# Kernel optimization log

Hardware: AMD Instinct MI355X
Metric: run time of the kernel (lower is better)

Reference implementation:

```python
import jax, jax.numpy as jnp
import numpy as np

B, U, H, M, D = 64, 1024, 16, 512, 4  # batch, units, numheads, memsize, depth
HS = U // H  # headsize


def setup_inputs() -> dict:
    key = jax.random.key(0)
    ks = jax.random.split(key, 6)
    scale = 0.02
    return {
        "x": jax.random.normal(ks[0], (B, U), jnp.float32),
        "memory": jax.random.normal(ks[1], (B, M * U), jnp.float32),
        "Wr": jax.random.normal(ks[2], (D, U, H * (M + 1)), jnp.float32) * scale,
        "br": jnp.zeros((D, H * (M + 1)), jnp.float32),
        "Ww": jax.random.normal(ks[3], (D, U, H * M), jnp.float32) * scale,
        "bw": jnp.zeros((D, H * M), jnp.float32),
        "Wk": jax.random.normal(ks[4], (D, U, U), jnp.float32) * scale,
        "bk": jnp.zeros((D, U), jnp.float32),
    }


def reference(x, memory, Wr, br, Ww, bw, Wk, bk):
    b = x.shape[0]
    mem4 = memory.reshape(b, M, H, HS)          # [B, M, H, HS]
    out = x
    for l in range(D):  # fixed small depth loop over structurally distinct layers
        inp4 = out.reshape(b, 1, H, HS)
        att = jnp.concatenate([mem4, inp4], axis=1)        # [B, M+1, H, HS]
        memstate = att.reshape(b, M + 1, U).mean(axis=1)   # [B, U]
        # read attention: per-head softmax over memory slots (+input slot)
        rlog = memstate @ Wr[l] + br[l]                    # [B, H*(M+1)]
        rw = jax.nn.softmax(rlog.reshape(b, M + 1, H), axis=1)  # [B, M+1, H]
        att = att * rw[..., None]                          # weighted read
        newval = jax.nn.relu(att.reshape(b, M + 1, U).sum(axis=1) @ Wk[l] + bk[l])  # [B, U]
        # write attention: per-head softmax over memory slots
        wlog = newval @ Ww[l] + bw[l]                      # [B, H*M]
        ww = jax.nn.softmax(wlog.reshape(b, M, H), axis=1)[..., None]  # [B, M, H, 1]
        mem4 = (1.0 - ww) * mem4 + ww * newval.reshape(b, 1, H, HS)
        out = newval
    return out, mem4.reshape(b, M * U)
```

## Files before the change

kernel.cpp:

```cpp
#include <hip/hip_runtime.h>

#define BB 64
#define UU 1024
#define HH 16
#define MM 512
#define DD 4
#define NR 8208
#define NW 8192
#define NK 1024

__device__ inline float warp_reduce_max(float v) {
    #pragma unroll
    for (int off = 32; off > 0; off >>= 1) v = fmaxf(v, __shfl_xor(v, off));
    return v;
}
__device__ inline float warp_reduce_sum(float v) {
    #pragma unroll
    for (int off = 32; off > 0; off >>= 1) v += __shfl_xor(v, off);
    return v;
}

__global__ void k_zero(float* __restrict__ p) {
    p[blockIdx.x * 256 + threadIdx.x] = 0.0f;
}

__global__ __launch_bounds__(256) void k_memsum(const float* __restrict__ mem,
                                                float* __restrict__ memsum) {
    const int b = blockIdx.x, mc = blockIdx.y, t = threadIdx.x;
    const float4* src = (const float4*)(mem + (size_t)b * MM * UU);
    float4 s = make_float4(0.f, 0.f, 0.f, 0.f);
    const int m0 = mc * 32;
    for (int m = m0; m < m0 + 32; ++m) {
        float4 v = src[(size_t)m * 256 + t];
        s.x += v.x; s.y += v.y; s.z += v.z; s.w += v.w;
    }
    float* d = memsum + b * UU + t * 4;
    atomicAdd(d + 0, s.x); atomicAdd(d + 1, s.y);
    atomicAdd(d + 2, s.z); atomicAdd(d + 3, s.w);
}

__global__ void k_prep_r(const float* __restrict__ memsum, const float* __restrict__ out,
                         float* __restrict__ memstate, float* __restrict__ wsum) {
    int i = blockIdx.x * 256 + threadIdx.x;
    memstate[i] = (memsum[i] + out[i]) * (1.0f / 513.0f);
    wsum[i] = 0.0f;
}

__global__ __launch_bounds__(256) void k_gemm(const float* __restrict__ A,
                                              const float* __restrict__ W,
                                              float* __restrict__ pbuf,
                                              int N, int kchunk, int kcl2 ) {
    __shared__ float At[256 * 64];
    const int t = threadIdx.x;
    const int cb = blockIdx.x * 128;
    const int ks = blockIdx.y;
    const int kbase = ks * kchunk;

    const int n4 = kchunk >> 4;
    const int kq_mask = (kchunk >> 2) - 1;
    for (int i = 0; i < n4; ++i) {
        int idx4 = t + (i << 8);
        int r = idx4 >> kcl2;
        int kq = idx4 & kq_mask;
        float4 v = *(const float4*)(A + r * UU + kbase + (kq << 2));
        int kk = kq << 2;
        At[(kk + 0) * 64 + r] = v.x;
        At[(kk + 1) * 64 + r] = v.y;
        At[(kk + 2) * 64 + r] = v.z;
        At[(kk + 3) * 64 + r] = v.w;
    }
    __syncthreads();

    const int wave = t >> 6;
    const int lane = t & 63;
    const int row0 = wave << 4;
    const int col = cb + (lane << 1);
    const bool wvalid = (col + 2 <= N);
    const float* Wp = W + (size_t)kbase * N + col;

    float acc[16][2];
    #pragma unroll
    for (int r = 0; r < 16; ++r) { acc[r][0] = 0.f; acc[r][1] = 0.f; }

    float2 wb0[8], wb1[8];
    if (wvalid) {
        #pragma unroll
        for (int i = 0; i < 8; ++i) wb0[i] = *(const float2*)(Wp + (size_t)i * N);
    }
    for (int kb = 0; kb < kchunk; kb += 8) {
        if (wvalid && (kb + 8 < kchunk)) {
            #pragma unroll
            for (int i = 0; i < 8; ++i)
                wb1[i] = *(const float2*)(Wp + (size_t)(kb + 8 + i) * N);
        }
        #pragma unroll
        for (int i = 0; i < 8; ++i) {
            const float* ap = &At[(kb + i) * 64 + row0];
            float a[16];
            *(float4*)&a[0]  = *(const float4*)(ap + 0);
            *(float4*)&a[4]  = *(const float4*)(ap + 4);
            *(float4*)&a[8]  = *(const float4*)(ap + 8);
            *(float4*)&a[12] = *(const float4*)(ap + 12);
            float2 wv = wb0[i];
            #pragma unroll
            for (int r = 0; r < 16; ++r) {
                acc[r][0] = fmaf(a[r], wv.x, acc[r][0]);
                acc[r][1] = fmaf(a[r], wv.y, acc[r][1]);
            }
        }
        #pragma unroll
        for (int i = 0; i < 8; ++i) wb0[i] = wb1[i];
    }

    if (wvalid) {
        float* dst = pbuf + (size_t)ks * 64 * N + col;
        #pragma unroll
        for (int r = 0; r < 16; ++r) {
            float2 o; o.x = acc[r][0]; o.y = acc[r][1];
            *(float2*)(dst + (size_t)(row0 + r) * N) = o;
        }
    }
}

__global__ __launch_bounds__(256) void k_softmax(const float* __restrict__ pbuf,
                                                 const float* __restrict__ bias,
                                                 float* __restrict__ outT,
                                                 int N, int S, int ksplit) {
    __shared__ float sm[4];
    const int b = blockIdx.x >> 4;
    const int h = blockIdx.x & 15;
    const int t = threadIdx.x;

    float v[3];
    float mx = -1e30f;
    #pragma unroll
    for (int i = 0; i < 3; ++i) {
        int slot = t + (i << 8);
        float val = -1e30f;
        if (slot < S) {
            int j = slot * HH + h;
            val = bias[j];
            for (int ks = 0; ks < ksplit; ++ks)
                val += pbuf[(size_t)(ks * BB + b) * N + j];
        }
        v[i] = val;
        mx = fmaxf(mx, val);
    }
    mx = warp_reduce_max(mx);
    if ((t & 63) == 0) sm[t >> 6] = mx;
    __syncthreads();
    mx = fmaxf(fmaxf(sm[0], sm[1]), fmaxf(sm[2], sm[3]));
    __syncthreads();

    float sum = 0.f;
    #pragma unroll
    for (int i = 0; i < 3; ++i) {
        int slot = t + (i << 8);
        if (slot < S) { v[i] = __expf(v[i] - mx); sum += v[i]; }
    }
    sum = warp_reduce_sum(sum);
    if ((t & 63) == 0) sm[t >> 6] = sum;
    __syncthreads();
    sum = sm[0] + sm[1] + sm[2] + sm[3];
    const float inv = 1.0f / sum;
    #pragma unroll
    for (int i = 0; i < 3; ++i) {
        int slot = t + (i << 8);
        if (slot < S) outT[(size_t)(b * HH + h) * S + slot] = v[i] * inv;
    }
}

__global__ __launch_bounds__(256) void k_passA(const float* __restrict__ mem,
                                               const float* __restrict__ rwT,
                                               float* __restrict__ wsum) {
    const int b = blockIdx.x, mc = blockIdx.y, t = threadIdx.x;
    const int h = t >> 4;
    const float4* src = (const float4*)(mem + (size_t)b * MM * UU);
    const float* rw = rwT + (size_t)(b * HH + h) * (MM + 1);
    float4 s = make_float4(0.f, 0.f, 0.f, 0.f);
    const int m0 = mc * 32;
    for (int m = m0; m < m0 + 32; ++m) {
        float wgt = rw[m];
        float4 v = src[(size_t)m * 256 + t];
        s.x = fmaf(wgt, v.x, s.x); s.y = fmaf(wgt, v.y, s.y);
        s.z = fmaf(wgt, v.z, s.z); s.w = fmaf(wgt, v.w, s.w);
    }
    float* d = wsum + b * UU + t * 4;
    atomicAdd(d + 0, s.x); atomicAdd(d + 1, s.y);
    atomicAdd(d + 2, s.z); atomicAdd(d + 3, s.w);
}

__global__ void k_prep_k(const float* __restrict__ wsum, const float* __restrict__ out,
                         const float* __restrict__ rwT, float* __restrict__ kin) {
    int i = blockIdx.x * 256 + threadIdx.x;
    int b = i >> 10, u = i & 1023;
    int h = u >> 6;
    float r = rwT[(size_t)(b * HH + h) * (MM + 1) + MM];
    kin[i] = fmaf(out[i], r, wsum[i]);
}

__global__ void k_relu(const float* __restrict__ pbuf, const float* __restrict__ bk,
                       float* __restrict__ newval, float* __restrict__ memsum,
                       float* __restrict__ outdst) {
    int i = blockIdx.x * 256 + threadIdx.x;
    int b = i >> 10, u = i & 1023;
    float v = bk[u];
    for (int ks = 0; ks < 32; ++ks) v += pbuf[(size_t)(ks * BB + b) * NK + u];
    v = fmaxf(v, 0.f);
    newval[i] = v;
    memsum[i] = 0.f;
    if (outdst) outdst[i] = v;
}

__global__ __launch_bounds__(256) void k_update(const float* __restrict__ src,
                                                float* __restrict__ dst,
                                                const float* __restrict__ wwT,
                                                const float* __restrict__ newval,
                                                float* __restrict__ memsum, int do_sum) {
    const int b = blockIdx.x, mc = blockIdx.y, t = threadIdx.x;
    const int h = t >> 4;
    const float4* s4 = (const float4*)(src + (size_t)b * MM * UU);
    float4* d4 = (float4*)(dst + (size_t)b * MM * UU);
    const float* ww = wwT + (size_t)(b * HH + h) * MM;
    float4 nv = *(const float4*)(newval + b * UU + t * 4);
    float4 acc = make_float4(0.f, 0.f, 0.f, 0.f);
    const int m0 = mc * 32;
    for (int m = m0; m < m0 + 32; ++m) {
        float wgt = ww[m];
        float4 v = s4[(size_t)m * 256 + t];
        v.x = fmaf(wgt, nv.x - v.x, v.x);
        v.y = fmaf(wgt, nv.y - v.y, v.y);
        v.z = fmaf(wgt, nv.z - v.z, v.z);
        v.w = fmaf(wgt, nv.w - v.w, v.w);
        d4[(size_t)m * 256 + t] = v;
        acc.x += v.x; acc.y += v.y; acc.z += v.z; acc.w += v.w;
    }
    if (do_sum) {
        float* d = memsum + b * UU + t * 4;
        atomicAdd(d + 0, acc.x); atomicAdd(d + 1, acc.y);
        atomicAdd(d + 2, acc.z); atomicAdd(d + 3, acc.w);
    }
}

extern "C" void kernel_launch(void* const* d_in, const int* in_sizes, int n_in,
                              void* d_out, int out_size, void* d_ws, size_t ws_size,
                              hipStream_t stream) {
    const float* x    = (const float*)d_in[0];
    const float* memI = (const float*)d_in[1];
    const float* Wr   = (const float*)d_in[2];
    const float* br   = (const float*)d_in[3];
    const float* Ww   = (const float*)d_in[4];
    const float* bw   = (const float*)d_in[5];
    const float* Wk   = (const float*)d_in[6];
    const float* bk   = (const float*)d_in[7];

    float* outp   = (float*)d_out;
    float* memOut = outp + BB * UU;

    char* w = (char*)d_ws;
    float* pbuf     = (float*)(w + 0);
    float* rwT      = (float*)(w + 8404992);
    float* wwT      = (float*)(w + 10506240);
    float* memsum   = (float*)(w + 12603392);
    float* wsum     = (float*)(w + 12865536);
    float* memstate = (float*)(w + 13127680);
    float* kin      = (float*)(w + 13389824);
    float* nv0      = (float*)(w + 13651968);
    float* nv1      = (float*)(w + 13914112);

    k_zero<<<BB * UU / 256, 256, 0, stream>>>(memsum);
    k_memsum<<<dim3(BB, 16), 256, 0, stream>>>(memI, memsum);

    const float* curOut = x;
    const float* curMem = memI;
    for (int l = 0; l < DD; ++l) {
        float* nv = (l & 1) ? nv1 : nv0;
        k_prep_r<<<BB * UU / 256, 256, 0, stream>>>(memsum, curOut, memstate, wsum);
        k_gemm<<<dim3(65, 4), 256, 0, stream>>>(memstate, Wr + (size_t)l * UU * NR, pbuf, NR, 256, 6);
        k_softmax<<<BB * HH, 256, 0, stream>>>(pbuf, br + (size_t)l * NR, rwT, NR, MM + 1, 4);
        k_passA<<<dim3(BB, 16), 256, 0, stream>>>(curMem, rwT, wsum);
        k_prep_k<<<BB * UU / 256, 256, 0, stream>>>(wsum, curOut, rwT, kin);
        k_gemm<<<dim3(8, 32), 256, 0, stream>>>(kin, Wk + (size_t)l * UU * NK, pbuf, NK, 32, 3);
        k_relu<<<BB * UU / 256, 256, 0, stream>>>(pbuf, bk + (size_t)l * NK, nv, memsum,
                                                  (l == DD - 1) ? outp : (float*)nullptr);
        k_gemm<<<dim3(64, 4), 256, 0, stream>>>(nv, Ww + (size_t)l * UU * NW, pbuf, NW, 256, 6);
        k_softmax<<<BB * HH, 256, 0, stream>>>(pbuf, bw + (size_t)l * NW, wwT, NW, MM, 4);
        k_update<<<dim3(BB, 16), 256, 0, stream>>>(curMem, memOut, wwT, nv, memsum,
                                                   (l < DD - 1) ? 1 : 0);
        curMem = memOut;
        curOut = nv;
    }
}
```

Measured before the change: 1.140 ms.

## Express memory state algebraically via write-weight products, defer memory materialization to final pass

Rewrites the per-layer memory update as a closed form: the memory after layer l is the original memory scaled by a product of (1-ww) factors plus a weighted sum of earlier newval vectors. Read sums and memory-state sums become weighted passes over the original input memory, with the newval terms folded into the GEMM A-operand load. The full memory tensor is written only once, in a final kernel, and pbuf plus the partial sums are staged in the output buffer. This drops the per-layer memory write traffic and the atomics, and uses more split-K for the large GEMMs. In exchange it adds more workspace, more per-element work in the softmax and GEMM prologues, and changes the floating-point rounding order.

```diff
diff --git a/kernel.cpp b/kernel.cpp
--- a/kernel.cpp
+++ b/kernel.cpp
@@ -8,6 +8,11 @@
 #define NR 8208
 #define NW 8192
 #define NK 1024
+#define BH  (BB * HH)
+#define BHM (BB * HH * MM)
+#define BU  (BB * UU)
+#define MCC 16
+
 
 __device__ inline float warp_reduce_max(float v) {
     #pragma unroll
@@ -20,37 +25,40 @@
     return v;
 }
 
-__global__ void k_zero(float* __restrict__ p) {
-    p[blockIdx.x * 256 + threadIdx.x] = 0.0f;
-}
-
-__global__ __launch_bounds__(256) void k_memsum(const float* __restrict__ mem,
-                                                float* __restrict__ memsum) {
+__global__ __launch_bounds__(256) void k_cpass(const float* __restrict__ mem,
+                                               const float* __restrict__ wt,
+                                               float* __restrict__ part) {
     const int b = blockIdx.x, mc = blockIdx.y, t = threadIdx.x;
+    const int h = t >> 4;
     const float4* src = (const float4*)(mem + (size_t)b * MM * UU);
     float4 s = make_float4(0.f, 0.f, 0.f, 0.f);
     const int m0 = mc * 32;
-    for (int m = m0; m < m0 + 32; ++m) {
-        float4 v = src[(size_t)m * 256 + t];
-        s.x += v.x; s.y += v.y; s.z += v.z; s.w += v.w;
-    }
-    float* d = memsum + b * UU + t * 4;
-    atomicAdd(d + 0, s.x); atomicAdd(d + 1, s.y);
-    atomicAdd(d + 2, s.z); atomicAdd(d + 3, s.w);
-}
-
-__global__ void k_prep_r(const float* __restrict__ memsum, const float* __restrict__ out,
-                         float* __restrict__ memstate, float* __restrict__ wsum) {
-    int i = blockIdx.x * 256 + threadIdx.x;
-    memstate[i] = (memsum[i] + out[i]) * (1.0f / 513.0f);
-    wsum[i] = 0.0f;
-}
-
-__global__ __launch_bounds__(256) void k_gemm(const float* __restrict__ A,
+    if (wt) {
+        const float* w = wt + (size_t)(b * HH + h) * MM;
+        for (int m = m0; m < m0 + 32; ++m) {
+            float g = w[m];
+            float4 v = src[(size_t)m * 256 + t];
+            s.x = fmaf(g, v.x, s.x); s.y = fmaf(g, v.y, s.y);
+            s.z = fmaf(g, v.z, s.z); s.w = fmaf(g, v.w, s.w);
+        }
+    } else {
+        for (int m = m0; m < m0 + 32; ++m) {
+            float4 v = src[(size_t)m * 256 + t];
+            s.x += v.x; s.y += v.y; s.z += v.z; s.w += v.w;
+        }
+    }
+    *(float4*)(part + ((size_t)(mc * BB + b) << 10) + t * 4) = s;
+}
+
+__global__ __launch_bounds__(256) void k_gemm(const float* __restrict__ Abase,
+                                              const float* __restrict__ parts,
+                                              const float* __restrict__ coefs, int ncoef,
+                                              const float* __restrict__ nvall,
+                                              const float* __restrict__ gvec, float scale,
                                               const float* __restrict__ W,
                                               float* __restrict__ pbuf,
-                                              int N, int kchunk, int kcl2 ) {
-    __shared__ float At[256 * 64];
+                                              int N, int kchunk, int kcl2) {
+    extern __shared__ float At[];
     const int t = threadIdx.x;
     const int cb = blockIdx.x * 128;
     const int ks = blockIdx.y;
@@ -62,7 +70,27 @@
         int idx4 = t + (i << 8);
         int r = idx4 >> kcl2;
         int kq = idx4 & kq_mask;
-        float4 v = *(const float4*)(A + r * UU + kbase + (kq << 2));
+        int u = kbase + (kq << 2);
+        float4 v;
+        if (parts) {
+            float4 o = *(const float4*)(Abase + r * UU + u);
+            const int h = u >> 6;
+            float g = gvec ? gvec[r * HH + h] : 1.0f;
+            v.x = g * o.x; v.y = g * o.y; v.z = g * o.z; v.w = g * o.w;
+            for (int mc = 0; mc < MCC; ++mc) {
+                const float4 p = *(const float4*)(parts + ((size_t)(mc * BB + r) << 10) + u);
+                v.x += p.x; v.y += p.y; v.z += p.z; v.w += p.w;
+            }
+            for (int j = 0; j < ncoef; ++j) {
+                float c = coefs[j * BH + r * HH + h];
+                const float4 nv = *(const float4*)(nvall + ((size_t)(j * BB + r) << 10) + u);
+                v.x = fmaf(c, nv.x, v.x); v.y = fmaf(c, nv.y, v.y);
+                v.z = fmaf(c, nv.z, v.z); v.w = fmaf(c, nv.w, v.w);
+            }
+            v.x *= scale; v.y *= scale; v.z *= scale; v.w *= scale;
+        } else {
+            v = *(const float4*)(Abase + r * UU + u);
+        }
         int kk = kq << 2;
         At[(kk + 0) * 64 + r] = v.x;
         At[(kk + 1) * 64 + r] = v.y;
@@ -122,13 +150,17 @@
     }
 }
 
-__global__ __launch_bounds__(256) void k_softmax(const float* __restrict__ pbuf,
-                                                 const float* __restrict__ bias,
-                                                 float* __restrict__ outT,
-                                                 int N, int S, int ksplit) {
+template <int LP>
+__global__ __launch_bounds__(256) void k_softmaxR(const float* __restrict__ pbuf,
+                                                  const float* __restrict__ bias,
+                                                  const float* __restrict__ wwall,
+                                                  float* __restrict__ wtbl,
+                                                  float* __restrict__ rwM,
+                                                  float* __restrict__ Rtab) {
     __shared__ float sm[4];
-    const int b = blockIdx.x >> 4;
-    const int h = blockIdx.x & 15;
+    __shared__ float sr[4][4];
+    const int bh = blockIdx.x;
+    const int b = bh >> 4, h = bh & 15;
     const int t = threadIdx.x;
 
     float v[3];
@@ -137,11 +169,11 @@
     for (int i = 0; i < 3; ++i) {
         int slot = t + (i << 8);
         float val = -1e30f;
-        if (slot < S) {
+        if (slot < MM + 1) {
             int j = slot * HH + h;
             val = bias[j];
-            for (int ks = 0; ks < ksplit; ++ks)
-                val += pbuf[(size_t)(ks * BB + b) * N + j];
+            #pragma unroll
+            for (int ks = 0; ks < 8; ++ks) val += pbuf[(size_t)(ks * BB + b) * NR + j];
         }
         v[i] = val;
         mx = fmaxf(mx, val);
@@ -156,89 +188,172 @@
     #pragma unroll
     for (int i = 0; i < 3; ++i) {
         int slot = t + (i << 8);
-        if (slot < S) { v[i] = __expf(v[i] - mx); sum += v[i]; }
+        if (slot < MM + 1) { v[i] = __expf(v[i] - mx); sum += v[i]; }
     }
     sum = warp_reduce_sum(sum);
     if ((t & 63) == 0) sm[t >> 6] = sum;
     __syncthreads();
     sum = sm[0] + sm[1] + sm[2] + sm[3];
     const float inv = 1.0f / sum;
-    #pragma unroll
-    for (int i = 0; i < 3; ++i) {
+
+    float racc[3] = {0.f, 0.f, 0.f};
+    #pragma unroll
+    for (int i = 0; i < 2; ++i) {
+        int m = t + (i << 8);
+        float p = v[i] * inv;
+        float prod = 1.f;
+        if (LP > 0) {
+            float w[3];
+            #pragma unroll
+            for (int j = 0; j < LP; ++j)
+                w[j] = wwall[((size_t)j * BH + bh) * MM + m];
+            #pragma unroll
+            for (int j = LP - 1; j >= 0; --j) {
+                racc[j] += p * (w[j] * prod);
+                prod *= (1.f - w[j]);
+            }
+        }
+        wtbl[(size_t)bh * MM + m] = p * prod;
+    }
+    if (t == 0) rwM[bh] = v[2] * inv;
+
+    if (LP > 0) {
+        #pragma unroll
+        for (int j = 0; j < LP; ++j) racc[j] = warp_reduce_sum(racc[j]);
+        if ((t & 63) == 0) {
+            #pragma unroll
+            for (int j = 0; j < LP; ++j) sr[t >> 6][j] = racc[j];
+        }
+        __syncthreads();
+        if (t < LP) Rtab[t * BH + bh] = sr[0][t] + sr[1][t] + sr[2][t] + sr[3][t];
+    }
+}
+
+template <int LP, int WSP>
+__global__ __launch_bounds__(256) void k_softmaxS(const float* __restrict__ pbuf,
+                                                  const float* __restrict__ bias,
+                                                  const float* __restrict__ wwall,
+                                                  float* __restrict__ wwOut,
+                                                  float* __restrict__ Pout,
+                                                  float* __restrict__ Stab) {
+    __shared__ float sm[4];
+    __shared__ float sr[4][4];
+    const int bh = blockIdx.x;
+    const int b = bh >> 4, h = bh & 15;
+    const int t = threadIdx.x;
+
+    float v[2];
+    float mx = -1e30f;
+    #pragma unroll
+    for (int i = 0; i < 2; ++i) {
         int slot = t + (i << 8);
-        if (slot < S) outT[(size_t)(b * HH + h) * S + slot] = v[i] * inv;
-    }
-}
-
-__global__ __launch_bounds__(256) void k_passA(const float* __restrict__ mem,
-                                               const float* __restrict__ rwT,
-                                               float* __restrict__ wsum) {
-    const int b = blockIdx.x, mc = blockIdx.y, t = threadIdx.x;
-    const int h = t >> 4;
-    const float4* src = (const float4*)(mem + (size_t)b * MM * UU);
-    const float* rw = rwT + (size_t)(b * HH + h) * (MM + 1);
-    float4 s = make_float4(0.f, 0.f, 0.f, 0.f);
-    const int m0 = mc * 32;
-    for (int m = m0; m < m0 + 32; ++m) {
-        float wgt = rw[m];
-        float4 v = src[(size_t)m * 256 + t];
-        s.x = fmaf(wgt, v.x, s.x); s.y = fmaf(wgt, v.y, s.y);
-        s.z = fmaf(wgt, v.z, s.z); s.w = fmaf(wgt, v.w, s.w);
-    }
-    float* d = wsum + b * UU + t * 4;
-    atomicAdd(d + 0, s.x); atomicAdd(d + 1, s.y);
-    atomicAdd(d + 2, s.z); atomicAdd(d + 3, s.w);
-}
-
-__global__ void k_prep_k(const float* __restrict__ wsum, const float* __restrict__ out,
-                         const float* __restrict__ rwT, float* __restrict__ kin) {
-    int i = blockIdx.x * 256 + threadIdx.x;
-    int b = i >> 10, u = i & 1023;
-    int h = u >> 6;
-    float r = rwT[(size_t)(b * HH + h) * (MM + 1) + MM];
-    kin[i] = fmaf(out[i], r, wsum[i]);
+        int j = slot * HH + h;
+        float val = bias[j];
+        #pragma unroll
+        for (int ks = 0; ks < 8; ++ks) val += pbuf[(size_t)(ks * BB + b) * NW + j];
+        v[i] = val;
+        mx = fmaxf(mx, val);
+    }
+    mx = warp_reduce_max(mx);
+    if ((t & 63) == 0) sm[t >> 6] = mx;
+    __syncthreads();
+    mx = fmaxf(fmaxf(sm[0], sm[1]), fmaxf(sm[2], sm[3]));
+    __syncthreads();
+
+    float sum = 0.f;
+    #pragma unroll
+    for (int i = 0; i < 2; ++i) { v[i] = __expf(v[i] - mx); sum += v[i]; }
+    sum = warp_reduce_sum(sum);
+    if ((t & 63) == 0) sm[t >> 6] = sum;
+    __syncthreads();
+    sum = sm[0] + sm[1] + sm[2] + sm[3];
+    const float inv = 1.0f / sum;
+
+    float sacc[4] = {0.f, 0.f, 0.f, 0.f};
+    #pragma unroll
+    for (int i = 0; i < 2; ++i) {
+        int m = t + (i << 8);
+        float p = v[i] * inv;
+        wwOut[(size_t)bh * MM + m] = p;
+        if (WSP) {
+            float prod = 1.f;
+            float q[3];
+            if (LP > 0) {
+                float w[3];
+                #pragma unroll
+                for (int j = 0; j < LP; ++j)
+                    w[j] = wwall[((size_t)j * BH + bh) * MM + m];
+                #pragma unroll
+                for (int j = LP - 1; j >= 0; --j) {
+                    q[j] = w[j] * prod;
+                    prod *= (1.f - w[j]);
+                }
+            }
+            float om = 1.f - p;
+            #pragma unroll
+            for (int j = 0; j < LP; ++j) sacc[j] += q[j] * om;
+            sacc[LP] += p;
+            Pout[(size_t)bh * MM + m] = prod * om;
+        }
+    }
+    if (WSP) {
+        #pragma unroll
+        for (int j = 0; j <= LP; ++j) sacc[j] = warp_reduce_sum(sacc[j]);
+        if ((t & 63) == 0) {
+            #pragma unroll
+            for (int j = 0; j <= LP; ++j) sr[t >> 6][j] = sacc[j];
+        }
+        __syncthreads();
+        if (t <= LP) Stab[t * BH + bh] = sr[0][t] + sr[1][t] + sr[2][t] + sr[3][t];
+    }
 }
 
 __global__ void k_relu(const float* __restrict__ pbuf, const float* __restrict__ bk,
-                       float* __restrict__ newval, float* __restrict__ memsum,
-                       float* __restrict__ outdst) {
+                       float* __restrict__ newval, float* __restrict__ outdst) {
     int i = blockIdx.x * 256 + threadIdx.x;
     int b = i >> 10, u = i & 1023;
     float v = bk[u];
     for (int ks = 0; ks < 32; ++ks) v += pbuf[(size_t)(ks * BB + b) * NK + u];
     v = fmaxf(v, 0.f);
     newval[i] = v;
-    memsum[i] = 0.f;
     if (outdst) outdst[i] = v;
 }
 
-__global__ __launch_bounds__(256) void k_update(const float* __restrict__ src,
-                                                float* __restrict__ dst,
-                                                const float* __restrict__ wwT,
-                                                const float* __restrict__ newval,
-                                                float* __restrict__ memsum, int do_sum) {
+__global__ __launch_bounds__(256) void k_final(const float* __restrict__ mem0,
+                                               const float* __restrict__ wwall,
+                                               const float* __restrict__ nvall,
+                                               float* __restrict__ dst) {
     const int b = blockIdx.x, mc = blockIdx.y, t = threadIdx.x;
     const int h = t >> 4;
-    const float4* s4 = (const float4*)(src + (size_t)b * MM * UU);
+    const float4* s4 = (const float4*)(mem0 + (size_t)b * MM * UU);
     float4* d4 = (float4*)(dst + (size_t)b * MM * UU);
-    const float* ww = wwT + (size_t)(b * HH + h) * MM;
-    float4 nv = *(const float4*)(newval + b * UU + t * 4);
-    float4 acc = make_float4(0.f, 0.f, 0.f, 0.f);
+    const float* w0 = wwall + ((size_t)(0 * BB + b) * HH + h) * MM;
+    const float* w1 = wwall + ((size_t)(1 * BB + b) * HH + h) * MM;
+    const float* w2 = wwall + ((size_t)(2 * BB + b) * HH + h) * MM;
+    const float* w3 = wwall + ((size_t)(3 * BB + b) * HH + h) * MM;
+    float4 n0 = *(const float4*)(nvall + ((size_t)(0 * BB + b) << 10) + t * 4);
+    float4 n1 = *(const float4*)(nvall + ((size_t)(1 * BB + b) << 10) + t * 4);
+    float4 n2 = *(const float4*)(nvall + ((size_t)(2 * BB + b) << 10) + t * 4);
+    float4 n3 = *(const float4*)(nvall + ((size_t)(3 * BB + b) << 10) + t * 4);
     const int m0 = mc * 32;
     for (int m = m0; m < m0 + 32; ++m) {
-        float wgt = ww[m];
+        float a0 = w0[m], a1 = w1[m], a2 = w2[m], a3 = w3[m];
+        float c3 = a3,        r3 = 1.f - a3;
+        float c2 = a2 * r3,   r2 = (1.f - a2) * r3;
+        float c1 = a1 * r2,   r1 = (1.f - a1) * r2;
+        float c0 = a0 * r1,   p  = (1.f - a0) * r1;
         float4 v = s4[(size_t)m * 256 + t];
-        v.x = fmaf(wgt, nv.x - v.x, v.x);
-        v.y = fmaf(wgt, nv.y - v.y, v.y);
-        v.z = fmaf(wgt, nv.z - v.z, v.z);
-        v.w = fmaf(wgt, nv.w - v.w, v.w);
-        d4[(size_t)m * 256 + t] = v;
-        acc.x += v.x; acc.y += v.y; acc.z += v.z; acc.w += v.w;
-    }
-    if (do_sum) {
-        float* d = memsum + b * UU + t * 4;
-        atomicAdd(d + 0, acc.x); atomicAdd(d + 1, acc.y);
-        atomicAdd(d + 2, acc.z); atomicAdd(d + 3, acc.w);
+        float4 o;
+        o.x = p * v.x; o.y = p * v.y; o.z = p * v.z; o.w = p * v.w;
+        o.x = fmaf(c0, n0.x, o.x); o.y = fmaf(c0, n0.y, o.y);
+        o.z = fmaf(c0, n0.z, o.z); o.w = fmaf(c0, n0.w, o.w);
+        o.x = fmaf(c1, n1.x, o.x); o.y = fmaf(c1, n1.y, o.y);
+        o.z = fmaf(c1, n1.z, o.z); o.w = fmaf(c1, n1.w, o.w);
+        o.x = fmaf(c2, n2.x, o.x); o.y = fmaf(c2, n2.y, o.y);
+        o.z = fmaf(c2, n2.z, o.z); o.w = fmaf(c2, n2.w, o.w);
+        o.x = fmaf(c3, n3.x, o.x); o.y = fmaf(c3, n3.y, o.y);
+        o.z = fmaf(c3, n3.z, o.z); o.w = fmaf(c3, n3.w, o.w);
+        d4[(size_t)m * 256 + t] = o;
     }
 }
 
@@ -257,37 +372,52 @@
     float* outp   = (float*)d_out;
     float* memOut = outp + BB * UU;
 
-    char* w = (char*)d_ws;
-    float* pbuf     = (float*)(w + 0);
-    float* rwT      = (float*)(w + 8404992);
-    float* wwT      = (float*)(w + 10506240);
-    float* memsum   = (float*)(w + 12603392);
-    float* wsum     = (float*)(w + 12865536);
-    float* memstate = (float*)(w + 13127680);
-    float* kin      = (float*)(w + 13389824);
-    float* nv0      = (float*)(w + 13651968);
-    float* nv1      = (float*)(w + 13914112);
-
-    k_zero<<<BB * UU / 256, 256, 0, stream>>>(memsum);
-    k_memsum<<<dim3(BB, 16), 256, 0, stream>>>(memI, memsum);
-
-    const float* curOut = x;
-    const float* curMem = memI;
+    float* wwAll = (float*)d_ws;
+    float* wtbl  = wwAll + 4 * BHM;
+    float* Ptbl  = wtbl + BHM;
+    float* nvAll = Ptbl + BHM;
+    float* rwM   = nvAll + 4 * BU;
+    float* Rtab  = rwM + BH;
+    float* Stab  = Rtab + 4 * BH;
+
+    float* pbuf  = memOut;
+    float* wcolp = pbuf + 8 * BB * NR;
+    float* rp    = wcolp + MCC * BU;
+
+    k_cpass<<<dim3(BB, MCC), 256, 0, stream>>>(memI, nullptr, wcolp);
+
     for (int l = 0; l < DD; ++l) {
-        float* nv = (l & 1) ? nv1 : nv0;
-        k_prep_r<<<BB * UU / 256, 256, 0, stream>>>(memsum, curOut, memstate, wsum);
-        k_gemm<<<dim3(65, 4), 256, 0, stream>>>(memstate, Wr + (size_t)l * UU * NR, pbuf, NR, 256, 6);
-        k_softmax<<<BB * HH, 256, 0, stream>>>(pbuf, br + (size_t)l * NR, rwT, NR, MM + 1, 4);
-        k_passA<<<dim3(BB, 16), 256, 0, stream>>>(curMem, rwT, wsum);
-        k_prep_k<<<BB * UU / 256, 256, 0, stream>>>(wsum, curOut, rwT, kin);
-        k_gemm<<<dim3(8, 32), 256, 0, stream>>>(kin, Wk + (size_t)l * UU * NK, pbuf, NK, 32, 3);
-        k_relu<<<BB * UU / 256, 256, 0, stream>>>(pbuf, bk + (size_t)l * NK, nv, memsum,
-                                                  (l == DD - 1) ? outp : (float*)nullptr);
-        k_gemm<<<dim3(64, 4), 256, 0, stream>>>(nv, Ww + (size_t)l * UU * NW, pbuf, NW, 256, 6);
-        k_softmax<<<BB * HH, 256, 0, stream>>>(pbuf, bw + (size_t)l * NW, wwT, NW, MM, 4);
-        k_update<<<dim3(BB, 16), 256, 0, stream>>>(curMem, memOut, wwT, nv, memsum,
-                                                   (l < DD - 1) ? 1 : 0);
-        curMem = memOut;
-        curOut = nv;
-    }
-}
+        const float* curOut = (l == 0) ? x : nvAll + (size_t)(l - 1) * BU;
+        float* nv = nvAll + (size_t)l * BU;
+        float* wwOut = wwAll + (size_t)l * BHM;
+
+        k_gemm<<<dim3(65, 8), 256, 128 * 64 * 4, stream>>>(
+            curOut, wcolp, Stab, l, nvAll, nullptr, 1.0f / 513.0f,
+            Wr + (size_t)l * UU * NR, pbuf, NR, 128, 5);
+        switch (l) {
+            case 0: k_softmaxR<0><<<BH, 256, 0, stream>>>(pbuf, br + (size_t)l * NR, wwAll, wtbl, rwM, Rtab); break;
+            case 1: k_softmaxR<1><<<BH, 256, 0, stream>>>(pbuf, br + (size_t)l * NR, wwAll, wtbl, rwM, Rtab); break;
+            case 2: k_softmaxR<2><<<BH, 256, 0, stream>>>(pbuf, br + (size_t)l * NR, wwAll, wtbl, rwM, Rtab); break;
+            default: k_softmaxR<3><<<BH, 256, 0, stream>>>(pbuf, br + (size_t)l * NR, wwAll, wtbl, rwM, Rtab); break;
+        }
+        k_cpass<<<dim3(BB, MCC), 256, 0, stream>>>(memI, wtbl, rp);
+        k_gemm<<<dim3(8, 32), 256, 32 * 64 * 4, stream>>>(
+            curOut, rp, Rtab, l, nvAll, rwM, 1.0f,
+            Wk + (size_t)l * UU * NK, pbuf, NK, 32, 3);
+        k_relu<<<BU / 256, 256, 0, stream>>>(pbuf, bk + (size_t)l * NK, nv,
+                                             (l == DD - 1) ? outp : (float*)nullptr);
+        k_gemm<<<dim3(64, 8), 256, 128 * 64 * 4, stream>>>(
+            nv, nullptr, nullptr, 0, nullptr, nullptr, 1.0f,
+            Ww + (size_t)l * UU * NW, pbuf, NW, 128, 5);
+        switch (l) {
+            case 0: k_softmaxS<0, 1><<<BH, 256, 0, stream>>>(pbuf, bw + (size_t)l * NW, wwAll, wwOut, Ptbl, Stab); break;
+            case 1: k_softmaxS<1, 1><<<BH, 256, 0, stream>>>(pbuf, bw + (size_t)l * NW, wwAll, wwOut, Ptbl, Stab); break;
+            case 2: k_softmaxS<2, 1><<<BH, 256, 0, stream>>>(pbuf, bw + (size_t)l * NW, wwAll, wwOut, Ptbl, Stab); break;
+            default: k_softmaxS<3, 0><<<BH, 256, 0, stream>>>(pbuf, bw + (size_t)l * NW, wwAll, wwOut, Ptbl, Stab); break;
+        }
+        if (l < DD - 1)
+            k_cpass<<<dim3(BB, MCC), 256, 0, stream>>>(memI, Ptbl, wcolp);
+    }
+
+    k_final<<<dim3(BB, 16), 256, 0, stream>>>(memI, wwAll, nvAll, memOut);
+}
```

Result: faster. 1.075 ms (-5.7%).
